# Performance work log

Hardware: AMD Instinct MI355X
Metric: run time of the kernel (lower is better)

## Reference

```python
import jax, jax.numpy as jnp
import numpy as np

B = 4096          # batch == in_features (required by the module's broadcast)
F = 4096          # in_features
OUT = 4096        # out_features


def _pairwise_l2(x):
    # torch.cdist(x, x, p=2): exact pairwise Euclidean distances [B, B]
    sq = jnp.sum(x * x, axis=-1)                       # [B]
    d2 = sq[:, None] + sq[None, :] - 2.0 * (x @ x.T)   # [B, B]
    d2 = jnp.maximum(d2, 0.0)
    # safe sqrt: zero distance (diagonal) -> 0 with zero subgradient
    d = jnp.sqrt(jnp.where(d2 > 0.0, d2, 1.0))
    return jnp.where(d2 > 0.0, d, 0.0)


def setup_inputs() -> dict:
    key = jax.random.key(0)
    k1, k2, k3, k4 = jax.random.split(key, 4)
    x = jax.random.normal(k1, (B, F), dtype=jnp.float32)
    # nn.Linear default init: U(-1/sqrt(fan_in), 1/sqrt(fan_in))
    lim_rbf = 1.0 / np.sqrt(F)
    lim_out = 1.0 / np.sqrt(F)
    W_rbf = jax.random.uniform(k2, (F, F), minval=-lim_rbf, maxval=lim_rbf, dtype=jnp.float32)
    W_out = jax.random.uniform(k3, (OUT, F), minval=-lim_out, maxval=lim_out, dtype=jnp.float32)
    b_out = jax.random.uniform(k4, (OUT,), minval=-lim_out, maxval=lim_out, dtype=jnp.float32)
    return {"x": x, "W_rbf": W_rbf, "W_out": W_out, "b_out": b_out}


def reference(x, W_rbf, W_out, b_out):
    dist = _pairwise_l2(x)                    # [B, B]
    gram = jnp.exp(-jnp.abs(W_rbf) * dist)    # [B, B] (B == F so broadcast is elementwise)
    mixed = gram @ x                          # [B, F]
    return mixed @ W_out.T + b_out            # [B, OUT]
```

## Files before the change

### kernel.cpp

```cpp
#include <hip/hip_runtime.h>
#include <cstdint>

#define LDD 4096
#define NT 64

typedef __attribute__((ext_vector_type(8))) short short8;
typedef __attribute__((ext_vector_type(4))) float f32x4;

__device__ __forceinline__ short f2bf(float f) {
  uint32_t u = __builtin_bit_cast(uint32_t, f);
  u += 0x7fffu + ((u >> 16) & 1u);
  return (short)(u >> 16);
}

__device__ __forceinline__ void async16(const void* g, void* l) {
  __builtin_amdgcn_global_load_lds(
      (const __attribute__((address_space(1))) unsigned*)(uintptr_t)g,
      (__attribute__((address_space(3))) unsigned*)(uintptr_t)l,
      16, 0, 0);
}

__global__ __launch_bounds__(256)
void prep_rows(const float* __restrict__ x, short* __restrict__ xb,
               float* __restrict__ sq) {
  int row = blockIdx.x, tid = threadIdx.x;
  const float4* xr = (const float4*)(x + (size_t)row * LDD);
  short4* xo = (short4*)(xb + (size_t)row * LDD);
  float s = 0.f;
#pragma unroll
  for (int i = 0; i < 4; i++) {
    float4 v = xr[i * 256 + tid];
    s = fmaf(v.x, v.x, s); s = fmaf(v.y, v.y, s);
    s = fmaf(v.z, v.z, s); s = fmaf(v.w, v.w, s);
    short4 o; o.x = f2bf(v.x); o.y = f2bf(v.y); o.z = f2bf(v.z); o.w = f2bf(v.w);
    xo[i * 256 + tid] = o;
  }
#pragma unroll
  for (int off = 32; off > 0; off >>= 1) s += __shfl_down(s, off, 64);
  __shared__ float red[4];
  int lane = tid & 63, wv = tid >> 6;
  if (lane == 0) red[wv] = s;
  __syncthreads();
  if (tid == 0) sq[row] = red[0] + red[1] + red[2] + red[3];
}

__global__ __launch_bounds__(256)
void transpose_bf16(const float* __restrict__ x, short* __restrict__ xT) {
  __shared__ float tile[64][65];
  int bx = blockIdx.x, by = blockIdx.y, tid = threadIdx.x;
  int tr = tid >> 4;
  int tc = (tid & 15) << 2;
#pragma unroll
  for (int i = 0; i < 4; i++) {
    int r = i * 16 + tr;
    float4 v = *(const float4*)(x + (size_t)(by * 64 + r) * LDD + bx * 64 + tc);
    tile[r][tc + 0] = v.x; tile[r][tc + 1] = v.y;
    tile[r][tc + 2] = v.z; tile[r][tc + 3] = v.w;
  }
  __syncthreads();
#pragma unroll
  for (int i = 0; i < 4; i++) {
    int fr = i * 16 + tr;
    short4 o;
    o.x = f2bf(tile[tc + 0][fr]); o.y = f2bf(tile[tc + 1][fr]);
    o.z = f2bf(tile[tc + 2][fr]); o.w = f2bf(tile[tc + 3][fr]);
    *(short4*)(xT + (size_t)(bx * 64 + fr) * LDD + by * 64 + tc) = o;
  }
}

__global__ __launch_bounds__(256)
void conv_bf16(const float* __restrict__ w, short* __restrict__ wb) {
  int i = blockIdx.x * 256 + threadIdx.x;
  float4 v = ((const float4*)w)[i];
  short4 o; o.x = f2bf(v.x); o.y = f2bf(v.y); o.z = f2bf(v.z); o.w = f2bf(v.w);
  ((short4*)wb)[i] = o;
}

#define SB() __builtin_amdgcn_sched_barrier(0)
#define LGKM(n) do { asm volatile("s_waitcnt lgkmcnt(" #n ")" ::: "memory"); SB(); } while (0)

template <int MODE>
__global__ __launch_bounds__(512, 2)
void gemm256(const short* __restrict__ A, const short* __restrict__ Bt,
             short* __restrict__ outB, float* __restrict__ outF,
             const float* __restrict__ extra, const float* __restrict__ sq) {
  __shared__ __attribute__((aligned(16))) char smem[131072];
  const int tid = threadIdx.x;

  int bid = blockIdx.x;
  int lin = (bid & 7) * 32 + (bid >> 3);
  const int rb = (lin >> 4) * 256;
  const int cb = (lin & 15) * 256;

  const int s0 = tid, s1 = 512 + tid;
  const int r0 = s0 >> 3, c0 = (s0 & 7) ^ (r0 & 7);
  const int r1 = s1 >> 3, c1 = (s1 & 7) ^ (r1 & 7);
  const size_t go0 = (size_t)r0 * LDD + (size_t)(c0 << 3);
  const size_t go1 = (size_t)r1 * LDD + (size_t)(c1 << 3);

  const short* gB0 = Bt + (size_t)cb * LDD;
  const short* gB1 = Bt + (size_t)(cb + 128) * LDD;
  const short* gA0 = A + (size_t)rb * LDD;
  const short* gA1 = A + (size_t)(rb + 128) * LDD;
  char* lst = smem + tid * 16;

  auto stage = [&](const short* g, int tt, int half) {
    const short* gp = g + (size_t)tt * 64;
    char* l = lst + ((tt & 1) << 16) + (half << 14);
    async16(gp + go0, l);
    async16(gp + go1, l + 8192);
  };

  const int lane = tid & 63;
  const int wv = tid >> 6;
  const int wm = wv >> 2;
  const int wn = wv & 3;
  const int fr = lane & 15;
  const int fq = lane >> 4;
  const int arow = fr * 128;
  const int brow = ((wn & 1) * 64 + fr) * 128;
  const int sx0 = ((fq ^ (fr & 7)) << 4);
  const int sx1 = (((4 + fq) ^ (fr & 7)) << 4);
  const int abase = 32768 + (wm << 14);
  const int bbase = (wn >> 1) << 14;

  f32x4 acc[8][4];
#pragma unroll
  for (int m = 0; m < 8; ++m)
#pragma unroll
    for (int n = 0; n < 4; ++n) acc[m][n] = {0.f, 0.f, 0.f, 0.f};

#define RD_AV(dst, base_off, ap)                                        \
  do {                                                                  \
    dst[0][0] = *(const short8*)((ap) + (base_off) + arow + sx0);       \
    dst[0][1] = *(const short8*)((ap) + (base_off) + arow + sx1);       \
    dst[1][0] = *(const short8*)((ap) + (base_off) + 2048 + arow + sx0);\
    dst[1][1] = *(const short8*)((ap) + (base_off) + 2048 + arow + sx1);\
  } while (0)

#define MM(av2, mb)                                                     \
  do {                                                                  \
    __builtin_amdgcn_s_setprio(1);                                      \
    _Pragma("unroll")                                                   \
    for (int kk = 0; kk < 2; ++kk)                                      \
      _Pragma("unroll")                                                 \
      for (int mi = 0; mi < 2; ++mi)                                    \
        _Pragma("unroll")                                               \
        for (int n = 0; n < 4; ++n)                                     \
          acc[(mb) + mi][n] = __builtin_amdgcn_mfma_f32_16x16x32_bf16(  \
              av2[mi][kk], bv[n][kk], acc[(mb) + mi][n], 0, 0, 0);      \
    __builtin_amdgcn_s_setprio(0);                                      \
  } while (0)

  short8 avX[2][2], avY[2][2], bv[4][2];

  stage(gB0, 0, 0); stage(gB1, 0, 1); stage(gA0, 0, 2); stage(gA1, 0, 3);
  stage(gB0, 1, 0); stage(gB1, 1, 1);
  asm volatile("s_waitcnt vmcnt(4)" ::: "memory");
  __builtin_amdgcn_s_barrier();
  RD_AV(avX, 0, smem + abase);
  SB();

  for (int t = 0; t < NT; ++t) {
    const int bufo = (t & 1) << 16;
    const char* ab = smem + bufo + abase;
    const char* bb = smem + bufo + bbase;
    const char* abn = smem + (bufo ^ (1 << 16)) + abase;

#pragma unroll
    for (int n = 0; n < 4; ++n) {
      bv[n][0] = *(const short8*)(bb + brow + n * 2048 + sx0);
      bv[n][1] = *(const short8*)(bb + brow + n * 2048 + sx1);
    }
    SB();
    RD_AV(avY, 4096, ab);
    SB();
    if (t + 1 < NT) stage(gA0, t + 1, 2);
    LGKM(4);
    __builtin_amdgcn_s_barrier();
    MM(avX, 0);

    RD_AV(avX, 8192, ab);
    SB();
    if (t + 1 < NT) stage(gA1, t + 1, 3);
    LGKM(4);
    MM(avY, 2);

    RD_AV(avY, 8192 + 4096, ab);
    SB();
    if (t + 2 < NT) stage(gB0, t + 2, 0);
    LGKM(4);
    MM(avX, 4);

    if (t + 2 < NT) stage(gB1, t + 2, 1);
    LGKM(0);
    if (t + 2 < NT) asm volatile("s_waitcnt vmcnt(4)" ::: "memory");
    else            asm volatile("s_waitcnt vmcnt(0)" ::: "memory");
    __builtin_amdgcn_s_barrier();
    if (t + 1 < NT) { RD_AV(avX, 0, abn); }
    SB();
    MM(avY, 6);
  }

  const int orow = rb + wm * 128 + fq * 4;
  const int ocol = cb + wn * 64 + fr;
  if (MODE == 0) {
    float sqc[4];
#pragma unroll
    for (int n = 0; n < 4; ++n) sqc[n] = sq[ocol + n * 16];
#pragma unroll
    for (int m = 0; m < 8; ++m) {
#pragma unroll
      for (int rr = 0; rr < 4; ++rr) {
        int row = orow + m * 16 + rr;
        float sqr = sq[row];
#pragma unroll
        for (int n = 0; n < 4; ++n) {
          size_t idx = (size_t)row * LDD + ocol + n * 16;
          float d2 = sqr + sqc[n] - 2.0f * acc[m][n][rr];
          float d = sqrtf(fmaxf(d2, 0.f));
          outB[idx] = f2bf(__expf(-fabsf(extra[idx]) * d));
        }
      }
    }
  } else if (MODE == 1) {
#pragma unroll
    for (int m = 0; m < 8; ++m)
#pragma unroll
      for (int rr = 0; rr < 4; ++rr) {
        int row = orow + m * 16 + rr;
#pragma unroll
        for (int n = 0; n < 4; ++n)
          outB[(size_t)row * LDD + ocol + n * 16] = f2bf(acc[m][n][rr]);
      }
  } else {
    float bc[4];
#pragma unroll
    for (int n = 0; n < 4; ++n) bc[n] = extra[ocol + n * 16];
#pragma unroll
    for (int m = 0; m < 8; ++m)
#pragma unroll
      for (int rr = 0; rr < 4; ++rr) {
        int row = orow + m * 16 + rr;
#pragma unroll
        for (int n = 0; n < 4; ++n)
          outF[(size_t)row * LDD + ocol + n * 16] = acc[m][n][rr] + bc[n];
      }
  }
#undef RD_AV
#undef MM
}

extern "C" void kernel_launch(void* const* d_in, const int* in_sizes, int n_in,
                              void* d_out, int out_size, void* d_ws, size_t ws_size,
                              hipStream_t stream) {
  const float* x    = (const float*)d_in[0];
  const float* Wrbf = (const float*)d_in[1];
  const float* Wout = (const float*)d_in[2];
  const float* bout = (const float*)d_in[3];
  float* out = (float*)d_out;

  char* ws = (char*)d_ws;
  short* xb    = (short*)ws;
  float* sq    = (float*)(ws + (size_t)32 * 1024 * 1024);
  short* woutb = (short*)(ws + (size_t)32 * 1024 * 1024);
  short* gram  = (short*)d_out;
  short* xT    = (short*)((char*)d_out + (size_t)32 * 1024 * 1024);
  short* mixed = xb;

  prep_rows<<<LDD, 256, 0, stream>>>(x, xb, sq);
  transpose_bf16<<<dim3(64, 64), 256, 0, stream>>>(x, xT);
  gemm256<0><<<256, 512, 0, stream>>>(xb, xb, gram, nullptr, Wrbf, sq);
  gemm256<1><<<256, 512, 0, stream>>>(gram, xT, mixed, nullptr, nullptr, nullptr);
  conv_bf16<<<LDD * LDD / 4 / 256, 256, 0, stream>>>(Wout, woutb);
  gemm256<2><<<256, 512, 0, stream>>>(mixed, woutb, nullptr, out, bout, nullptr);
}
```

Before: 517.4 us.

## Switch GEMM inner loop from 16x16x32 to 32x32x16 bf16 MFMA tiles

Replaces the 16x16x32 MFMA fragments with 32x32x16 MFMA, so each wave holds a 4x2 grid of 32x32 accumulators instead of 8x4 16x16 ones. LDS fragment reads, swizzle offsets and the per-phase MFMA grouping are reorganized to the new K-slicing, and all three epilogues are rewritten for the 32x32 output lane mapping. The intent is fewer LDS reads per FLOP and fewer MFMA issues. The cost is higher per-instruction latency and a more complex output index mapping that must exactly match the hardware layout.

New measurement: 558.5 us. 7.9% more time.

```diff
diff --git a/kernel.cpp b/kernel.cpp
--- a/kernel.cpp
+++ b/kernel.cpp
@@ -5,7 +5,7 @@
 #define NT 64
 
 typedef __attribute__((ext_vector_type(8))) short short8;
-typedef __attribute__((ext_vector_type(4))) float f32x4;
+typedef __attribute__((ext_vector_type(16))) float f32x16;
 
 __device__ __forceinline__ short f2bf(float f) {
   uint32_t u = __builtin_bit_cast(uint32_t, f);
@@ -115,50 +115,51 @@
   const int wv = tid >> 6;
   const int wm = wv >> 2;
   const int wn = wv & 3;
-  const int fr = lane & 15;
-  const int fq = lane >> 4;
-  const int arow = fr * 128;
-  const int brow = ((wn & 1) * 64 + fr) * 128;
-  const int sx0 = ((fq ^ (fr & 7)) << 4);
-  const int sx1 = (((4 + fq) ^ (fr & 7)) << 4);
+  const int l31 = lane & 31;
+  const int lk = lane >> 5;
   const int abase = 32768 + (wm << 14);
   const int bbase = (wn >> 1) << 14;
-
-  f32x4 acc[8][4];
-#pragma unroll
-  for (int m = 0; m < 8; ++m)
-#pragma unroll
-    for (int n = 0; n < 4; ++n) acc[m][n] = {0.f, 0.f, 0.f, 0.f};
-
-#define RD_AV(dst, base_off, ap)                                        \
+  const int arow = l31 * 128;
+  const int brow = ((wn & 1) * 64 + l31) * 128;
+  int sx[4];
+#pragma unroll
+  for (int s = 0; s < 4; ++s) sx[s] = (((2 * s + lk) ^ (lane & 7)) << 4);
+
+  f32x16 acc[4][2];
+#pragma unroll
+  for (int mf = 0; mf < 4; ++mf)
+#pragma unroll
+    for (int nf = 0; nf < 2; ++nf)
+#pragma unroll
+      for (int e = 0; e < 16; ++e) acc[mf][nf][e] = 0.f;
+
+#define RD_AV(dst, sxv, ap)                                             \
   do {                                                                  \
-    dst[0][0] = *(const short8*)((ap) + (base_off) + arow + sx0);       \
-    dst[0][1] = *(const short8*)((ap) + (base_off) + arow + sx1);       \
-    dst[1][0] = *(const short8*)((ap) + (base_off) + 2048 + arow + sx0);\
-    dst[1][1] = *(const short8*)((ap) + (base_off) + 2048 + arow + sx1);\
+    dst[0] = *(const short8*)((ap) + arow + 0 * 4096 + (sxv));          \
+    dst[1] = *(const short8*)((ap) + arow + 1 * 4096 + (sxv));          \
+    dst[2] = *(const short8*)((ap) + arow + 2 * 4096 + (sxv));          \
+    dst[3] = *(const short8*)((ap) + arow + 3 * 4096 + (sxv));          \
   } while (0)
 
-#define MM(av2, mb)                                                     \
+#define MM(av4, s)                                                      \
   do {                                                                  \
     __builtin_amdgcn_s_setprio(1);                                      \
     _Pragma("unroll")                                                   \
-    for (int kk = 0; kk < 2; ++kk)                                      \
+    for (int mf = 0; mf < 4; ++mf)                                      \
       _Pragma("unroll")                                                 \
-      for (int mi = 0; mi < 2; ++mi)                                    \
-        _Pragma("unroll")                                               \
-        for (int n = 0; n < 4; ++n)                                     \
-          acc[(mb) + mi][n] = __builtin_amdgcn_mfma_f32_16x16x32_bf16(  \
-              av2[mi][kk], bv[n][kk], acc[(mb) + mi][n], 0, 0, 0);      \
+      for (int nf = 0; nf < 2; ++nf)                                    \
+        acc[mf][nf] = __builtin_amdgcn_mfma_f32_32x32x16_bf16(          \
+            av4[mf], bv[nf][s], acc[mf][nf], 0, 0, 0);                  \
     __builtin_amdgcn_s_setprio(0);                                      \
   } while (0)
 
-  short8 avX[2][2], avY[2][2], bv[4][2];
+  short8 avX[4], avY[4], bv[2][4];
 
   stage(gB0, 0, 0); stage(gB1, 0, 1); stage(gA0, 0, 2); stage(gA1, 0, 3);
   stage(gB0, 1, 0); stage(gB1, 1, 1);
   asm volatile("s_waitcnt vmcnt(4)" ::: "memory");
   __builtin_amdgcn_s_barrier();
-  RD_AV(avX, 0, smem + abase);
+  RD_AV(avX, sx[0], smem + abase);
   SB();
 
   for (int t = 0; t < NT; ++t) {
@@ -168,84 +169,93 @@
     const char* abn = smem + (bufo ^ (1 << 16)) + abase;
 
 #pragma unroll
-    for (int n = 0; n < 4; ++n) {
-      bv[n][0] = *(const short8*)(bb + brow + n * 2048 + sx0);
-      bv[n][1] = *(const short8*)(bb + brow + n * 2048 + sx1);
+    for (int s = 0; s < 4; ++s) {
+      bv[0][s] = *(const short8*)(bb + brow + 0 * 4096 + sx[s]);
+      bv[1][s] = *(const short8*)(bb + brow + 1 * 4096 + sx[s]);
     }
     SB();
-    RD_AV(avY, 4096, ab);
+    RD_AV(avY, sx[1], ab);
     SB();
     if (t + 1 < NT) stage(gA0, t + 1, 2);
     LGKM(4);
     __builtin_amdgcn_s_barrier();
     MM(avX, 0);
 
-    RD_AV(avX, 8192, ab);
+    RD_AV(avX, sx[2], ab);
     SB();
     if (t + 1 < NT) stage(gA1, t + 1, 3);
     LGKM(4);
-    MM(avY, 2);
-
-    RD_AV(avY, 8192 + 4096, ab);
+    MM(avY, 1);
+
+    RD_AV(avY, sx[3], ab);
     SB();
     if (t + 2 < NT) stage(gB0, t + 2, 0);
     LGKM(4);
-    MM(avX, 4);
+    MM(avX, 2);
 
     if (t + 2 < NT) stage(gB1, t + 2, 1);
     LGKM(0);
     if (t + 2 < NT) asm volatile("s_waitcnt vmcnt(4)" ::: "memory");
     else            asm volatile("s_waitcnt vmcnt(0)" ::: "memory");
     __builtin_amdgcn_s_barrier();
-    if (t + 1 < NT) { RD_AV(avX, 0, abn); }
-    SB();
-    MM(avY, 6);
-  }
-
-  const int orow = rb + wm * 128 + fq * 4;
-  const int ocol = cb + wn * 64 + fr;
+    if (t + 1 < NT) { RD_AV(avX, sx[0], abn); }
+    SB();
+    MM(avY, 3);
+  }
+
+  const int ocol0 = cb + (wn >> 1) * 128 + (wn & 1) * 64 + l31;
+  const int orow0 = rb + wm * 128 + lk * 4;
   if (MODE == 0) {
-    float sqc[4];
-#pragma unroll
-    for (int n = 0; n < 4; ++n) sqc[n] = sq[ocol + n * 16];
-#pragma unroll
-    for (int m = 0; m < 8; ++m) {
-#pragma unroll
-      for (int rr = 0; rr < 4; ++rr) {
-        int row = orow + m * 16 + rr;
-        float sqr = sq[row];
-#pragma unroll
-        for (int n = 0; n < 4; ++n) {
-          size_t idx = (size_t)row * LDD + ocol + n * 16;
-          float d2 = sqr + sqc[n] - 2.0f * acc[m][n][rr];
-          float d = sqrtf(fmaxf(d2, 0.f));
-          outB[idx] = f2bf(__expf(-fabsf(extra[idx]) * d));
+    float sqc[2];
+#pragma unroll
+    for (int nf = 0; nf < 2; ++nf) sqc[nf] = sq[ocol0 + nf * 32];
+#pragma unroll
+    for (int mf = 0; mf < 4; ++mf) {
+#pragma unroll
+      for (int eq = 0; eq < 4; ++eq) {
+#pragma unroll
+        for (int er = 0; er < 4; ++er) {
+          int row = orow0 + mf * 32 + er + 8 * eq;
+          float sqr = sq[row];
+#pragma unroll
+          for (int nf = 0; nf < 2; ++nf) {
+            size_t idx = (size_t)row * LDD + ocol0 + nf * 32;
+            float d2 = sqr + sqc[nf] - 2.0f * acc[mf][nf][eq * 4 + er];
+            float d = sqrtf(fmaxf(d2, 0.f));
+            outB[idx] = f2bf(__expf(-fabsf(extra[idx]) * d));
+          }
         }
       }
     }
   } else if (MODE == 1) {
 #pragma unroll
-    for (int m = 0; m < 8; ++m)
-#pragma unroll
-      for (int rr = 0; rr < 4; ++rr) {
-        int row = orow + m * 16 + rr;
-#pragma unroll
-        for (int n = 0; n < 4; ++n)
-          outB[(size_t)row * LDD + ocol + n * 16] = f2bf(acc[m][n][rr]);
-      }
+    for (int mf = 0; mf < 4; ++mf)
+#pragma unroll
+      for (int eq = 0; eq < 4; ++eq)
+#pragma unroll
+        for (int er = 0; er < 4; ++er) {
+          int row = orow0 + mf * 32 + er + 8 * eq;
+#pragma unroll
+          for (int nf = 0; nf < 2; ++nf)
+            outB[(size_t)row * LDD + ocol0 + nf * 32] =
+                f2bf(acc[mf][nf][eq * 4 + er]);
+        }
   } else {
-    float bc[4];
-#pragma unroll
-    for (int n = 0; n < 4; ++n) bc[n] = extra[ocol + n * 16];
-#pragma unroll
-    for (int m = 0; m < 8; ++m)
-#pragma unroll
-      for (int rr = 0; rr < 4; ++rr) {
-        int row = orow + m * 16 + rr;
-#pragma unroll
-        for (int n = 0; n < 4; ++n)
-          outF[(size_t)row * LDD + ocol + n * 16] = acc[m][n][rr] + bc[n];
-      }
+    float bc[2];
+#pragma unroll
+    for (int nf = 0; nf < 2; ++nf) bc[nf] = extra[ocol0 + nf * 32];
+#pragma unroll
+    for (int mf = 0; mf < 4; ++mf)
+#pragma unroll
+      for (int eq = 0; eq < 4; ++eq)
+#pragma unroll
+        for (int er = 0; er < 4; ++er) {
+          int row = orow0 + mf * 32 + er + 8 * eq;
+#pragma unroll
+          for (int nf = 0; nf < 2; ++nf)
+            outF[(size_t)row * LDD + ocol0 + nf * 32] =
+                acc[mf][nf][eq * 4 + er] + bc[nf];
+        }
   }
 #undef RD_AV
 #undef MM
```

## Fuse W_out bf16 conversion into mixing GEMM epilogue; transpose from bf16 rows

Applied to the files above, without the earlier changes.

The separate kernel that converts W_out to bf16 is removed. Each block of the second GEMM now converts its own slice of W_out after writing its output tile, saving one launch and aiming to overlap that memory traffic with the GEMM tail. The transpose kernel now reads the already-converted bf16 rows instead of the fp32 input, which halves its read traffic and drops the per-element rounding. The cost is a longer epilogue in the mixing GEMM, which may add to its critical path, since all blocks finish at roughly the same time.

After: 521.6 us. Within noise of the previous version (+0.8%).

```diff
diff --git a/kernel.cpp b/kernel.cpp
--- a/kernel.cpp
+++ b/kernel.cpp
@@ -45,35 +45,27 @@
 }
 
 __global__ __launch_bounds__(256)
-void transpose_bf16(const float* __restrict__ x, short* __restrict__ xT) {
-  __shared__ float tile[64][65];
+void transpose_b16(const short* __restrict__ xb, short* __restrict__ xT) {
+  __shared__ unsigned short tile[64][68];
   int bx = blockIdx.x, by = blockIdx.y, tid = threadIdx.x;
   int tr = tid >> 4;
   int tc = (tid & 15) << 2;
 #pragma unroll
   for (int i = 0; i < 4; i++) {
     int r = i * 16 + tr;
-    float4 v = *(const float4*)(x + (size_t)(by * 64 + r) * LDD + bx * 64 + tc);
-    tile[r][tc + 0] = v.x; tile[r][tc + 1] = v.y;
-    tile[r][tc + 2] = v.z; tile[r][tc + 3] = v.w;
+    short4 v = *(const short4*)(xb + (size_t)(by * 64 + r) * LDD + bx * 64 + tc);
+    tile[r][tc + 0] = (unsigned short)v.x; tile[r][tc + 1] = (unsigned short)v.y;
+    tile[r][tc + 2] = (unsigned short)v.z; tile[r][tc + 3] = (unsigned short)v.w;
   }
   __syncthreads();
 #pragma unroll
   for (int i = 0; i < 4; i++) {
     int fr = i * 16 + tr;
     short4 o;
-    o.x = f2bf(tile[tc + 0][fr]); o.y = f2bf(tile[tc + 1][fr]);
-    o.z = f2bf(tile[tc + 2][fr]); o.w = f2bf(tile[tc + 3][fr]);
+    o.x = (short)tile[tc + 0][fr]; o.y = (short)tile[tc + 1][fr];
+    o.z = (short)tile[tc + 2][fr]; o.w = (short)tile[tc + 3][fr];
     *(short4*)(xT + (size_t)(bx * 64 + fr) * LDD + by * 64 + tc) = o;
   }
-}
-
-__global__ __launch_bounds__(256)
-void conv_bf16(const float* __restrict__ w, short* __restrict__ wb) {
-  int i = blockIdx.x * 256 + threadIdx.x;
-  float4 v = ((const float4*)w)[i];
-  short4 o; o.x = f2bf(v.x); o.y = f2bf(v.y); o.z = f2bf(v.z); o.w = f2bf(v.w);
-  ((short4*)wb)[i] = o;
 }
 
 #define SB() __builtin_amdgcn_sched_barrier(0)
@@ -83,7 +75,8 @@
 __global__ __launch_bounds__(512, 2)
 void gemm256(const short* __restrict__ A, const short* __restrict__ Bt,
              short* __restrict__ outB, float* __restrict__ outF,
-             const float* __restrict__ extra, const float* __restrict__ sq) {
+             const float* __restrict__ extra, const float* __restrict__ sq,
+             const float* __restrict__ wsrc, short* __restrict__ wdst) {
   __shared__ __attribute__((aligned(16))) char smem[131072];
   const int tid = threadIdx.x;
 
@@ -233,6 +226,19 @@
         for (int n = 0; n < 4; ++n)
           outB[(size_t)row * LDD + ocol + n * 16] = f2bf(acc[m][n][rr]);
       }
+    {
+      const float4* srcv = (const float4*)wsrc;
+      short4* dstv = (short4*)wdst;
+      const int base = bid * (LDD * LDD / 4 / 256);
+#pragma unroll 4
+      for (int j = 0; j < 32; ++j) {
+        int idx = base + j * 512 + tid;
+        float4 v = srcv[idx];
+        short4 o; o.x = f2bf(v.x); o.y = f2bf(v.y);
+        o.z = f2bf(v.z); o.w = f2bf(v.w);
+        dstv[idx] = o;
+      }
+    }
   } else {
     float bc[4];
 #pragma unroll
@@ -269,9 +275,11 @@
   short* mixed = xb;
 
   prep_rows<<<LDD, 256, 0, stream>>>(x, xb, sq);
-  transpose_bf16<<<dim3(64, 64), 256, 0, stream>>>(x, xT);
-  gemm256<0><<<256, 512, 0, stream>>>(xb, xb, gram, nullptr, Wrbf, sq);
-  gemm256<1><<<256, 512, 0, stream>>>(gram, xT, mixed, nullptr, nullptr, nullptr);
-  conv_bf16<<<LDD * LDD / 4 / 256, 256, 0, stream>>>(Wout, woutb);
-  gemm256<2><<<256, 512, 0, stream>>>(mixed, woutb, nullptr, out, bout, nullptr);
-}
+  transpose_b16<<<dim3(64, 64), 256, 0, stream>>>(xb, xT);
+  gemm256<0><<<256, 512, 0, stream>>>(xb, xb, gram, nullptr, Wrbf, sq,
+                                      nullptr, nullptr);
+  gemm256<1><<<256, 512, 0, stream>>>(gram, xT, mixed, nullptr, nullptr, nullptr,
+                                      Wout, woutb);
+  gemm256<2><<<256, 512, 0, stream>>>(mixed, woutb, nullptr, out, bout, nullptr,
+                                      nullptr, nullptr);
+}
```
